# Kernel tuning notes

Measured on AMD Instinct MI355X. Metric: run time of the kernel, lower is better.

## Reference

```python
import jax, jax.numpy as jnp
import numpy as np

N_NODES = 20000

def _gcn_conv(x, W, b, src, dst, n):
    # PyG GCNConv: add self-loops, symmetric normalization D^-1/2 (A+I) D^-1/2, then XW + b
    h = x @ W                                   # [n, out]
    loop = jnp.arange(n, dtype=src.dtype)
    s = jnp.concatenate([src, loop])            # sources incl. self-loops
    d = jnp.concatenate([dst, loop])            # targets incl. self-loops
    deg = jax.ops.segment_sum(jnp.ones_like(d, dtype=h.dtype), d, num_segments=n)
    dinv = jnp.where(deg > 0, jax.lax.rsqrt(deg), 0.0)
    norm = dinv[s] * dinv[d]                    # [E+n]
    msg = h[s] * norm[:, None]                  # gather + scale
    out = jax.ops.segment_sum(msg, d, num_segments=n)  # scatter-add
    return out + b


def setup_inputs() -> dict:
    key = jax.random.key(0)
    ks = jax.random.split(key, 12)
    n, text_dim, hidden, ncls = N_NODES, 768, 128, 4
    mel_flat = 128 * 128
    E = 640000
    def lin(k, fan_in, fan_out):
        bound = 1.0 / np.sqrt(fan_in)
        kw, kb = jax.random.split(k)
        W = jax.random.uniform(kw, (fan_in, fan_out), jnp.float32, -bound, bound)
        b = jax.random.uniform(kb, (fan_out,), jnp.float32, -bound, bound)
        return W, b
    W_mel, b_mel = lin(ks[0], mel_flat, hidden)
    W_cat, b_cat = lin(ks[1], text_dim + hidden, hidden)
    W1, b1 = lin(ks[2], hidden, hidden)
    W2, b2 = lin(ks[3], hidden, ncls)
    return {
        "text": jax.random.normal(ks[4], (n, text_dim), jnp.float32),
        "mel": jax.random.normal(ks[5], (n, 128, 128), jnp.float32),
        "edge_index": jax.random.randint(ks[6], (2, E), 0, n, jnp.int32),
        "W_mel": W_mel, "b_mel": b_mel,
        "W_cat": W_cat, "b_cat": b_cat,
        "W1": W1, "b1": b1,
        "W2": W2, "b2": b2,
    }


def reference(text, mel, edge_index, W_mel, b_mel, W_cat, b_cat, W1, b1, W2, b2):
    n = text.shape[0]
    src, dst = edge_index[0], edge_index[1]
    m = mel.reshape(n, -1)                      # flatten [N, 128*128]
    m = jax.nn.relu(m @ W_mel + b_mel)          # [N, hidden]
    x = jnp.concatenate([text, m], axis=1)      # [N, text_dim + hidden]
    x = jax.nn.relu(x @ W_cat + b_cat)          # [N, hidden]
    x = jax.nn.relu(_gcn_conv(x, W1, b1, src, dst, n))
    x = _gcn_conv(x, W2, b2, src, dst, n)       # [N, num_classes]
    return x
```

## Files before the change

### kernel.cpp

```cpp
#include <hip/hip_runtime.h>
#include <hip/hip_bf16.h>
#include <cstdint>

typedef float f32x4 __attribute__((ext_vector_type(4)));
typedef __bf16 bf16x8 __attribute__((ext_vector_type(8)));
typedef __bf16 bf16x4 __attribute__((ext_vector_type(4)));
typedef __bf16 bf16x2 __attribute__((ext_vector_type(2)));

#define HID 128

__global__ void pack_all(const float* __restrict__ Wa, const float* __restrict__ Wb,
                         const float* __restrict__ Wc,
                         __bf16* __restrict__ Ba, __bf16* __restrict__ Bb,
                         __bf16* __restrict__ Bc) {
    int idx = blockIdx.x * 256 + threadIdx.x;
    const int T1 = 512 * 512;
    const int T2 = 28 * 512;
    const int T3 = 4 * 512;
    const float* W; __bf16* B; int li;
    if (idx < T1)            { W = Wa; B = Ba; li = idx; }
    else if (idx < T1 + T2)  { W = Wb; B = Bb; li = idx - T1; }
    else if (idx < T1 + T2 + T3) { W = Wc; B = Bc; li = idx - T1 - T2; }
    else return;
    int lane = li & 63;
    int nf = (li >> 6) & 7;
    int ki = li >> 9;
    int n = nf * 16 + (lane & 15);
    int kb = ki * 32 + ((lane >> 4) * 8);
    bf16x8 v;
#pragma unroll
    for (int j = 0; j < 8; ++j) v[j] = (__bf16)W[(size_t)(kb + j) * HID + n];
    *reinterpret_cast<bf16x8*>(B + (size_t)li * 8) = v;
}

__global__ __launch_bounds__(256, 2) void gemm_mel_ks(
    const float* __restrict__ A0,
    const __bf16* __restrict__ Bf,
    __bf16* __restrict__ part)
{
    const int tid = threadIdx.x;
    const int lane = tid & 63;
    const int wv = tid >> 6;
    const int quarter = blockIdx.x / 625;
    const int row_base = (blockIdx.x - quarter * 625) * 32;
    const int rif = lane & 15;
    const int kg = lane >> 4;
    const int s0 = quarter * 8;

    __shared__ __align__(16) char ldsb[65536];

    f32x4 zero = {0.f, 0.f, 0.f, 0.f};
    f32x4 acc[2][8];
#pragma unroll
    for (int i = 0; i < 2; ++i)
#pragma unroll
        for (int j = 0; j < 8; ++j) acc[i][j] = zero;

    const bf16x8* __restrict__ BfV = reinterpret_cast<const bf16x8*>(Bf);

    f32x4 st[16];

    auto stage_load = [&](int s) {
#pragma unroll
        for (int j = 0; j < 16; ++j) {
            int seg = wv * 16 + j;
            int row = seg >> 1, halfseg = seg & 1;
            const float* gp = A0 + (size_t)(row_base + row) * 16384 + s * 512 + halfseg * 256 + (lane << 2);
            st[j] = __builtin_nontemporal_load(reinterpret_cast<const f32x4*>(gp));
        }
    };
    auto stage_write = [&](int buf) {
#pragma unroll
        for (int j = 0; j < 16; ++j) {
            int seg = wv * 16 + j;
            int row = seg >> 1, halfseg = seg & 1;
            int byte = row * 1024 + ((halfseg * 512 + lane * 8) ^ ((row & 7) << 4)) + buf * 32768;
            bf16x4 v;
            v[0] = (__bf16)st[j][0]; v[1] = (__bf16)st[j][1];
            v[2] = (__bf16)st[j][2]; v[3] = (__bf16)st[j][3];
            *reinterpret_cast<bf16x4*>(ldsb + byte) = v;
        }
    };
    auto compute2 = [&](int cur, int s, int kt0) {
#pragma unroll
        for (int kt = kt0; kt < kt0 + 2; ++kt) {
            bf16x8 af[2];
#pragma unroll
            for (int mi = 0; mi < 2; ++mi) {
                int row = mi * 16 + rif;
                int byte = row * 1024 + ((wv * 256 + kt * 64 + kg * 16) ^ ((rif & 7) << 4)) + cur * 32768;
                af[mi] = *reinterpret_cast<const bf16x8*>(ldsb + byte);
            }
            int ki = s * 16 + wv * 4 + kt;
            const bf16x8* bp = BfV + (size_t)ki * 512 + lane;
#pragma unroll
            for (int nf = 0; nf < 8; ++nf) {
                bf16x8 b = bp[nf * 64];
                acc[0][nf] = __builtin_amdgcn_mfma_f32_16x16x32_bf16(af[0], b, acc[0][nf], 0, 0, 0);
                acc[1][nf] = __builtin_amdgcn_mfma_f32_16x16x32_bf16(af[1], b, acc[1][nf], 0, 0, 0);
            }
        }
    };

    stage_load(s0);
    stage_write(0);
    for (int t = 0; t < 8; ++t) {
        int s = s0 + t;
        int cur = t & 1;
        if (t + 1 < 8) stage_load(s + 1);
        __syncthreads();
        compute2(cur, s, 0);
        compute2(cur, s, 2);
        if (t + 1 < 8) stage_write(cur ^ 1);
    }

    __syncthreads();
    float* red = reinterpret_cast<float*>(ldsb);
#pragma unroll
    for (int mi = 0; mi < 2; ++mi)
#pragma unroll
        for (int nf = 0; nf < 8; ++nf)
#pragma unroll
            for (int j = 0; j < 4; ++j)
                red[(wv * 32 + mi * 16 + kg * 4 + j) * HID + nf * 16 + rif] = acc[mi][nf][j];
    __syncthreads();
    __bf16* pb = part + (size_t)quarter * 20000 * HID;
#pragma unroll
    for (int p = 0; p < 8; ++p) {
        int idx = tid + p * 256;
        int r = idx >> 6;
        int c2 = (idx & 63) * 2;
        float v0 = red[r * HID + c2]     + red[(32 + r) * HID + c2]
                 + red[(64 + r) * HID + c2] + red[(96 + r) * HID + c2];
        float v1 = red[r * HID + c2 + 1] + red[(32 + r) * HID + c2 + 1]
                 + red[(64 + r) * HID + c2 + 1] + red[(96 + r) * HID + c2 + 1];
        union { bf16x2 h; unsigned int u; } cv;
        cv.h[0] = (__bf16)v0; cv.h[1] = (__bf16)v1;
        __builtin_nontemporal_store(cv.u,
            reinterpret_cast<unsigned int*>(pb + (size_t)(row_base + r) * HID + c2));
    }
}

__global__ __launch_bounds__(256) void gemm_cat_h1(
    const float* __restrict__ A0,
    const __bf16* __restrict__ part,
    const float* __restrict__ bmel,
    const __bf16* __restrict__ Bf2,
    const __bf16* __restrict__ Bf3,
    const float* __restrict__ bcat,
    const float* __restrict__ dinv,
    __bf16* __restrict__ h1)
{
    const int tid = threadIdx.x;
    const int lane = tid & 63;
    const int w = tid >> 6;
    const int row_base = blockIdx.x * 32;
    const int rif = lane & 15;
    const int kg = lane >> 4;

    f32x4 zero = {0.f, 0.f, 0.f, 0.f};
    f32x4 acc[2][8];
#pragma unroll
    for (int i = 0; i < 2; ++i)
#pragma unroll
        for (int j = 0; j < 8; ++j) acc[i][j] = zero;

    const bf16x8* __restrict__ Bf2V = reinterpret_cast<const bf16x8*>(Bf2);
    const int kstart = w * 224;
    const size_t N = (size_t)20000 * HID;

#pragma unroll
    for (int it = 0; it < 7; ++it) {
        const int k0 = kstart + it * 32;
        const int kc = k0 + kg * 8;
        bf16x8 af[2];
#pragma unroll
        for (int mi = 0; mi < 2; ++mi) {
            const int row = row_base + mi * 16 + rif;
            if (k0 < 768) {
                const f32x4* apv = reinterpret_cast<const f32x4*>(A0 + (size_t)row * 768 + kc);
                f32x4 v0 = __builtin_nontemporal_load(apv);
                f32x4 v1 = __builtin_nontemporal_load(apv + 1);
                af[mi][0] = (__bf16)v0.x; af[mi][1] = (__bf16)v0.y;
                af[mi][2] = (__bf16)v0.z; af[mi][3] = (__bf16)v0.w;
                af[mi][4] = (__bf16)v1.x; af[mi][5] = (__bf16)v1.y;
                af[mi][6] = (__bf16)v1.z; af[mi][7] = (__bf16)v1.w;
            } else {
                const int mcol = kc - 768;
                const size_t base = (size_t)row * HID + mcol;
                bf16x8 q0 = *reinterpret_cast<const bf16x8*>(part + base);
                bf16x8 q1 = *reinterpret_cast<const bf16x8*>(part + N + base);
                bf16x8 q2 = *reinterpret_cast<const bf16x8*>(part + 2 * N + base);
                bf16x8 q3 = *reinterpret_cast<const bf16x8*>(part + 3 * N + base);
                const float* bp_ = bmel + mcol;
#pragma unroll
                for (int jj = 0; jj < 8; ++jj) {
                    float v = (float)q0[jj] + (float)q1[jj] + (float)q2[jj] + (float)q3[jj] + bp_[jj];
                    af[mi][jj] = (__bf16)fmaxf(v, 0.f);
                }
            }
        }
        const bf16x8* bp = Bf2V + (size_t)(k0 >> 5) * 512 + lane;
#pragma unroll
        for (int nf = 0; nf < 8; ++nf) {
            bf16x8 b = bp[nf * 64];
            acc[0][nf] = __builtin_amdgcn_mfma_f32_16x16x32_bf16(af[0], b, acc[0][nf], 0, 0, 0);
            acc[1][nf] = __builtin_amdgcn_mfma_f32_16x16x32_bf16(af[1], b, acc[1][nf], 0, 0, 0);
        }
    }

    __shared__ float red[4][32][HID];
    __shared__ __bf16 xs[32][136];

#pragma unroll
    for (int mi = 0; mi < 2; ++mi)
#pragma unroll
        for (int nf = 0; nf < 8; ++nf)
#pragma unroll
            for (int j = 0; j < 4; ++j)
                red[w][mi * 16 + kg * 4 + j][nf * 16 + rif] = acc[mi][nf][j];
    __syncthreads();
#pragma unroll
    for (int p = 0; p < 16; ++p) {
        int idx = tid + p * 256;
        int r = idx >> 7, c = idx & 127;
        float v = red[0][r][c] + red[1][r][c] + red[2][r][c] + red[3][r][c];
        v = fmaxf(v + bcat[c], 0.f);
        xs[r][c] = (__bf16)v;
    }
    __syncthreads();

    f32x4 acc2[2][8];
#pragma unroll
    for (int i = 0; i < 2; ++i)
#pragma unroll
        for (int j = 0; j < 8; ++j) acc2[i][j] = zero;

    {
        const int k0 = w * 32;
        bf16x8 af[2];
#pragma unroll
        for (int mi = 0; mi < 2; ++mi)
            af[mi] = *reinterpret_cast<const bf16x8*>(&xs[mi * 16 + rif][k0 + kg * 8]);
        const bf16x8* bp = reinterpret_cast<const bf16x8*>(Bf3) + (size_t)w * 512 + lane;
#pragma unroll
        for (int nf = 0; nf < 8; ++nf) {
            bf16x8 b = bp[nf * 64];
            acc2[0][nf] = __builtin_amdgcn_mfma_f32_16x16x32_bf16(af[0], b, acc2[0][nf], 0, 0, 0);
            acc2[1][nf] = __builtin_amdgcn_mfma_f32_16x16x32_bf16(af[1], b, acc2[1][nf], 0, 0, 0);
        }
    }

#pragma unroll
    for (int mi = 0; mi < 2; ++mi)
#pragma unroll
        for (int nf = 0; nf < 8; ++nf)
#pragma unroll
            for (int j = 0; j < 4; ++j)
                red[w][mi * 16 + kg * 4 + j][nf * 16 + rif] = acc2[mi][nf][j];
    __syncthreads();
#pragma unroll
    for (int p = 0; p < 16; ++p) {
        int idx = tid + p * 256;
        int r = idx >> 7, c = idx & 127;
        float v = red[0][r][c] + red[1][r][c] + red[2][r][c] + red[3][r][c];
        h1[(size_t)(row_base + r) * HID + c] = (__bf16)(v * dinv[row_base + r]);
    }
}

__global__ void count_dst(const int* __restrict__ dst, int* __restrict__ cnt, int E) {
    int e = blockIdx.x * 256 + threadIdx.x;
    if (e < E) atomicAdd(&cnt[dst[e]], 1);
}

__global__ __launch_bounds__(1024) void scan_block(const int* __restrict__ cnt,
    int* __restrict__ offs, float* __restrict__ dinv, int n) {
    int tid = threadIdx.x;
    int CH = (n + 1023) >> 10;
    int s0 = tid * CH;
    int s1 = min(s0 + CH, n);
    int sum = 0;
    for (int i = s0; i < s1; ++i) sum += cnt[i];
    int lane = tid & 63, wv = tid >> 6;
    int s = sum;
#pragma unroll
    for (int off = 1; off < 64; off <<= 1) {
        int t = __shfl_up(s, off);
        if (lane >= off) s += t;
    }
    __shared__ int wsum[16];
    __shared__ int wbase[16];
    if (lane == 63) wsum[wv] = s;
    __syncthreads();
    if (tid == 0) {
        int a = 0;
#pragma unroll
        for (int k = 0; k < 16; ++k) { wbase[k] = a; a += wsum[k]; }
        offs[n] = a;
    }
    __syncthreads();
    int run = wbase[wv] + (s - sum);
    for (int i = s0; i < s1; ++i) {
        int v = cnt[i];
        offs[i] = run;
        dinv[i] = rsqrtf((float)(v + 1));
        run += v;
    }
}

__global__ void fill_csr(const int* __restrict__ src, const int* __restrict__ dst,
                         const int* __restrict__ offs, int* __restrict__ cnt,
                         int* __restrict__ srcs, int E) {
    int e = blockIdx.x * 256 + threadIdx.x;
    if (e >= E) return;
    int d = dst[e];
    int p = offs[d] + atomicAdd(&cnt[d], -1) - 1;
    srcs[p] = src[e];
}

__global__ __launch_bounds__(64) void agg_h_w2(const __bf16* __restrict__ hs,
    const float* __restrict__ dinv, const int* __restrict__ offs,
    const int* __restrict__ srcs,
    const float* __restrict__ b1, const float* __restrict__ W2,
    float* __restrict__ h2, int n) {
    int i = blockIdx.x;
    int c = threadIdx.x;
    float di = dinv[i];
    const int col = 2 * c;
    bf16x2 hv = *reinterpret_cast<const bf16x2*>(hs + (size_t)i * HID + col);
    float a0 = (float)hv[0];
    float a1 = (float)hv[1];
    int o = offs[i];
    int e = offs[i + 1] - o;
    int t = 0;
    for (; t + 8 <= e; t += 8) {
        int sx[8];
#pragma unroll
        for (int q = 0; q < 8; ++q) sx[q] = srcs[o + t + q];
        bf16x2 v[8];
#pragma unroll
        for (int q = 0; q < 8; ++q) v[q] = *reinterpret_cast<const bf16x2*>(hs + (size_t)sx[q] * HID + col);
#pragma unroll
        for (int q = 0; q < 8; ++q) { a0 += (float)v[q][0]; a1 += (float)v[q][1]; }
    }
    for (; t < e; ++t) {
        int s = srcs[o + t];
        bf16x2 v = *reinterpret_cast<const bf16x2*>(hs + (size_t)s * HID + col);
        a0 += (float)v[0];
        a1 += (float)v[1];
    }
    float yb0 = fmaxf(a0 * di + b1[col], 0.f);
    float yb1 = fmaxf(a1 * di + b1[col + 1], 0.f);
    float4 w0 = *reinterpret_cast<const float4*>(W2 + col * 4);
    float4 w1 = *reinterpret_cast<const float4*>(W2 + col * 4 + 4);
    float p0 = yb0 * w0.x + yb1 * w1.x;
    float p1 = yb0 * w0.y + yb1 * w1.y;
    float p2 = yb0 * w0.z + yb1 * w1.z;
    float p3 = yb0 * w0.w + yb1 * w1.w;
#pragma unroll
    for (int off = 32; off; off >>= 1) {
        p0 += __shfl_down(p0, off);
        p1 += __shfl_down(p1, off);
        p2 += __shfl_down(p2, off);
        p3 += __shfl_down(p3, off);
    }
    if (c == 0) {
        float4 r = {p0 * di, p1 * di, p2 * di, p3 * di};
        *reinterpret_cast<float4*>(h2 + (size_t)i * 4) = r;
    }
}

__global__ void agg4(const float* __restrict__ h2s, const float* __restrict__ dinv,
                     const int* __restrict__ offs,
                     const int* __restrict__ srcs, const float* __restrict__ b2,
                     float* __restrict__ out, int n) {
    int gid = blockIdx.x * 256 + threadIdx.x;
    int i = gid >> 2;
    int c = gid & 3;
    if (i >= n) return;
    float di = dinv[i];
    float acc = h2s[(size_t)i * 4 + c];
    int o = offs[i];
    int e = offs[i + 1] - o;
    int t = 0;
    for (; t + 4 <= e; t += 4) {
        int a0 = srcs[o + t], a1 = srcs[o + t + 1], a2 = srcs[o + t + 2], a3 = srcs[o + t + 3];
        acc += h2s[(size_t)a0 * 4 + c] + h2s[(size_t)a1 * 4 + c]
             + h2s[(size_t)a2 * 4 + c] + h2s[(size_t)a3 * 4 + c];
    }
    for (; t < e; ++t) {
        int s = srcs[o + t];
        acc += h2s[(size_t)s * 4 + c];
    }
    out[(size_t)i * 4 + c] = acc * di + b2[c];
}

extern "C" void kernel_launch(void* const* d_in, const int* in_sizes, int n_in,
                              void* d_out, int out_size, void* d_ws, size_t ws_size,
                              hipStream_t stream) {
    const float* text = (const float*)d_in[0];
    const float* mel  = (const float*)d_in[1];
    const int*   ei   = (const int*)d_in[2];
    const float* Wmel = (const float*)d_in[3];
    const float* bmel = (const float*)d_in[4];
    const float* Wcat = (const float*)d_in[5];
    const float* bcat = (const float*)d_in[6];
    const float* W1   = (const float*)d_in[7];
    const float* b1   = (const float*)d_in[8];
    const float* W2   = (const float*)d_in[9];
    const float* b2   = (const float*)d_in[10];
    float* out = (float*)d_out;

    const int n = in_sizes[0] / 768;
    const int E = in_sizes[2] / 2;
    const int Kmel = 16384;

    char* ws = (char*)d_ws;
    size_t off = 0;
    auto alloc = [&](size_t bytes) {
        void* p = ws + off;
        off += (bytes + 255) & ~(size_t)255;
        return p;
    };
    __bf16* Bf1 = (__bf16*)alloc((size_t)Kmel * HID * 2);
    __bf16* Bf2 = (__bf16*)alloc((size_t)896 * HID * 2);
    __bf16* Bf3 = (__bf16*)alloc((size_t)HID * HID * 2);
    __bf16* part = (__bf16*)alloc((size_t)4 * n * HID * 2);
    __bf16* h1  = (__bf16*)alloc((size_t)n * HID * 2);
    float* h2   = (float*)alloc((size_t)n * 4 * 4);
    int* cnt    = (int*)alloc((size_t)n * 4);
    int* offs   = (int*)alloc((size_t)(n + 1) * 4);
    float* dinv = (float*)alloc((size_t)n * 4);
    int* srcs   = (int*)alloc((size_t)E * 4);
    (void)ws_size; (void)n_in; (void)out_size;

    const int* srcI = ei;
    const int* dstI = ei + E;

    (void)hipMemsetAsync(cnt, 0, n * 4, stream);
    count_dst<<<(E + 255) / 256, 256, 0, stream>>>(dstI, cnt, E);
    scan_block<<<1, 1024, 0, stream>>>(cnt, offs, dinv, n);
    fill_csr<<<(E + 255) / 256, 256, 0, stream>>>(srcI, dstI, offs, cnt, srcs, E);

    pack_all<<<1088, 256, 0, stream>>>(Wmel, Wcat, W1, Bf1, Bf2, Bf3);

    gemm_mel_ks<<<2500, 256, 0, stream>>>(mel, Bf1, part);
    gemm_cat_h1<<<n / 32, 256, 0, stream>>>(text, part, bmel, Bf2, Bf3, bcat, dinv, h1);
    agg_h_w2<<<n, 64, 0, stream>>>(h1, dinv, offs, srcs, b1, W2, h2, n);
    agg4<<<(n * 4 + 255) / 256, 256, 0, stream>>>(h2, dinv, offs, srcs, b2, out, n);
}
```

Measured before the change: 435.4 us.

## Fuse degree count into weight packing and CSR fill into mel GEMM

```diff
diff --git a/kernel.cpp b/kernel.cpp
--- a/kernel.cpp
+++ b/kernel.cpp
@@ -9,19 +9,23 @@
 
 #define HID 128
 
-__global__ void pack_all(const float* __restrict__ Wa, const float* __restrict__ Wb,
-                         const float* __restrict__ Wc,
-                         __bf16* __restrict__ Ba, __bf16* __restrict__ Bb,
-                         __bf16* __restrict__ Bc) {
-    int idx = blockIdx.x * 256 + threadIdx.x;
+__global__ void count_pack(const int* __restrict__ dstI, int* __restrict__ cnt, int E,
+                           const float* __restrict__ Wa, const float* __restrict__ Wb,
+                           const float* __restrict__ Wc,
+                           __bf16* __restrict__ Ba, __bf16* __restrict__ Bb,
+                           __bf16* __restrict__ Bc) {
+    if (blockIdx.x < 256) {
+        for (int e = blockIdx.x * 256 + threadIdx.x; e < E; e += 65536)
+            atomicAdd(&cnt[dstI[e]], 1);
+        return;
+    }
+    int idx = (blockIdx.x - 256) * 256 + threadIdx.x;
     const int T1 = 512 * 512;
     const int T2 = 28 * 512;
-    const int T3 = 4 * 512;
     const float* W; __bf16* B; int li;
     if (idx < T1)            { W = Wa; B = Ba; li = idx; }
     else if (idx < T1 + T2)  { W = Wb; B = Bb; li = idx - T1; }
-    else if (idx < T1 + T2 + T3) { W = Wc; B = Bc; li = idx - T1 - T2; }
-    else return;
+    else                     { W = Wc; B = Bc; li = idx - T1 - T2; }
     int lane = li & 63;
     int nf = (li >> 6) & 7;
     int ki = li >> 9;
@@ -33,16 +37,30 @@
     *reinterpret_cast<bf16x8*>(B + (size_t)li * 8) = v;
 }
 
-__global__ __launch_bounds__(256, 2) void gemm_mel_ks(
+__global__ __launch_bounds__(256, 2) void gemm_mel_fill(
     const float* __restrict__ A0,
     const __bf16* __restrict__ Bf,
-    __bf16* __restrict__ part)
+    __bf16* __restrict__ part,
+    const int* __restrict__ srcI, const int* __restrict__ dstI,
+    const int* __restrict__ offs, int* __restrict__ cnt,
+    int* __restrict__ srcs, int E)
 {
+    const int b = blockIdx.x;
+    if ((b % 11) == 10) {
+        int fid = b / 11;
+        for (int e = fid * 256 + threadIdx.x; e < E; e += 64000) {
+            int d = dstI[e];
+            int p = offs[d] + atomicAdd(&cnt[d], -1) - 1;
+            srcs[p] = srcI[e];
+        }
+        return;
+    }
+    const int bid = b - b / 11;
     const int tid = threadIdx.x;
     const int lane = tid & 63;
     const int wv = tid >> 6;
-    const int quarter = blockIdx.x / 625;
-    const int row_base = (blockIdx.x - quarter * 625) * 32;
+    const int quarter = bid / 625;
+    const int row_base = (bid - quarter * 625) * 32;
     const int rif = lane & 15;
     const int kg = lane >> 4;
     const int s0 = quarter * 8;
@@ -95,9 +113,9 @@
             const bf16x8* bp = BfV + (size_t)ki * 512 + lane;
 #pragma unroll
             for (int nf = 0; nf < 8; ++nf) {
-                bf16x8 b = bp[nf * 64];
-                acc[0][nf] = __builtin_amdgcn_mfma_f32_16x16x32_bf16(af[0], b, acc[0][nf], 0, 0, 0);
-                acc[1][nf] = __builtin_amdgcn_mfma_f32_16x16x32_bf16(af[1], b, acc[1][nf], 0, 0, 0);
+                bf16x8 bq = bp[nf * 64];
+                acc[0][nf] = __builtin_amdgcn_mfma_f32_16x16x32_bf16(af[0], bq, acc[0][nf], 0, 0, 0);
+                acc[1][nf] = __builtin_amdgcn_mfma_f32_16x16x32_bf16(af[1], bq, acc[1][nf], 0, 0, 0);
             }
         }
     };
@@ -203,9 +221,9 @@
         const bf16x8* bp = Bf2V + (size_t)(k0 >> 5) * 512 + lane;
 #pragma unroll
         for (int nf = 0; nf < 8; ++nf) {
-            bf16x8 b = bp[nf * 64];
-            acc[0][nf] = __builtin_amdgcn_mfma_f32_16x16x32_bf16(af[0], b, acc[0][nf], 0, 0, 0);
-            acc[1][nf] = __builtin_amdgcn_mfma_f32_16x16x32_bf16(af[1], b, acc[1][nf], 0, 0, 0);
+            bf16x8 bq = bp[nf * 64];
+            acc[0][nf] = __builtin_amdgcn_mfma_f32_16x16x32_bf16(af[0], bq, acc[0][nf], 0, 0, 0);
+            acc[1][nf] = __builtin_amdgcn_mfma_f32_16x16x32_bf16(af[1], bq, acc[1][nf], 0, 0, 0);
         }
     }
 
@@ -245,9 +263,9 @@
         const bf16x8* bp = reinterpret_cast<const bf16x8*>(Bf3) + (size_t)w * 512 + lane;
 #pragma unroll
         for (int nf = 0; nf < 8; ++nf) {
-            bf16x8 b = bp[nf * 64];
-            acc2[0][nf] = __builtin_amdgcn_mfma_f32_16x16x32_bf16(af[0], b, acc2[0][nf], 0, 0, 0);
-            acc2[1][nf] = __builtin_amdgcn_mfma_f32_16x16x32_bf16(af[1], b, acc2[1][nf], 0, 0, 0);
+            bf16x8 bq = bp[nf * 64];
+            acc2[0][nf] = __builtin_amdgcn_mfma_f32_16x16x32_bf16(af[0], bq, acc2[0][nf], 0, 0, 0);
+            acc2[1][nf] = __builtin_amdgcn_mfma_f32_16x16x32_bf16(af[1], bq, acc2[1][nf], 0, 0, 0);
         }
     }
 
@@ -266,11 +284,6 @@
         float v = red[0][r][c] + red[1][r][c] + red[2][r][c] + red[3][r][c];
         h1[(size_t)(row_base + r) * HID + c] = (__bf16)(v * dinv[row_base + r]);
     }
-}
-
-__global__ void count_dst(const int* __restrict__ dst, int* __restrict__ cnt, int E) {
-    int e = blockIdx.x * 256 + threadIdx.x;
-    if (e < E) atomicAdd(&cnt[dst[e]], 1);
 }
 
 __global__ __launch_bounds__(1024) void scan_block(const int* __restrict__ cnt,
@@ -306,16 +319,6 @@
         dinv[i] = rsqrtf((float)(v + 1));
         run += v;
     }
-}
-
-__global__ void fill_csr(const int* __restrict__ src, const int* __restrict__ dst,
-                         const int* __restrict__ offs, int* __restrict__ cnt,
-                         int* __restrict__ srcs, int E) {
-    int e = blockIdx.x * 256 + threadIdx.x;
-    if (e >= E) return;
-    int d = dst[e];
-    int p = offs[d] + atomicAdd(&cnt[d], -1) - 1;
-    srcs[p] = src[e];
 }
 
 __global__ __launch_bounds__(64) void agg_h_w2(const __bf16* __restrict__ hs,
@@ -438,13 +441,9 @@
     const int* dstI = ei + E;
 
     (void)hipMemsetAsync(cnt, 0, n * 4, stream);
-    count_dst<<<(E + 255) / 256, 256, 0, stream>>>(dstI, cnt, E);
+    count_pack<<<1344, 256, 0, stream>>>(dstI, cnt, E, Wmel, Wcat, W1, Bf1, Bf2, Bf3);
     scan_block<<<1, 1024, 0, stream>>>(cnt, offs, dinv, n);
-    fill_csr<<<(E + 255) / 256, 256, 0, stream>>>(srcI, dstI, offs, cnt, srcs, E);
-
-    pack_all<<<1088, 256, 0, stream>>>(Wmel, Wcat, W1, Bf1, Bf2, Bf3);
-
-    gemm_mel_ks<<<2500, 256, 0, stream>>>(mel, Bf1, part);
+    gemm_mel_fill<<<2750, 256, 0, stream>>>(mel, Bf1, part, srcI, dstI, offs, cnt, srcs, E);
     gemm_cat_h1<<<n / 32, 256, 0, stream>>>(text, part, bmel, Bf2, Bf3, bcat, dinv, h1);
     agg_h_w2<<<n, 64, 0, stream>>>(h1, dinv, offs, srcs, b1, W2, h2, n);
     agg4<<<(n * 4 + 255) / 256, 256, 0, stream>>>(h2, dinv, offs, srcs, b2, out, n);
```

Result: faster. 420.8 us (median of 2 runs) (-3.4%).
